# Optimization experiments

Measured on AMD Instinct MI355X. Metric: run time of the kernel, lower is better.

The kernel has to match this reference:

```python
import jax, jax.numpy as jnp
import numpy as np

LN_EPS = 1e-5

def _layer_norm(y):
    # elementwise_affine=False LayerNorm over last dim
    mu = jnp.mean(y, axis=-1, keepdims=True)
    var = jnp.var(y, axis=-1, keepdims=True)
    return (y - mu) / jnp.sqrt(var + LN_EPS)

def setup_inputs() -> dict:
    key = jax.random.key(0)
    k0, k1, k2, k3, k4 = jax.random.split(key, 5)
    N, D, D_qk, D_v, n_out = 8192, 1024, 128, 1024, 1024
    w_std = 0.02
    x = jax.random.normal(k0, (N, D), dtype=jnp.float32)
    Wq = jax.random.normal(k1, (D_qk, D), dtype=jnp.float32) * w_std
    Wk = jax.random.normal(k2, (D_qk, D), dtype=jnp.float32) * w_std
    Wv = jax.random.normal(k3, (D_v, D), dtype=jnp.float32) * w_std
    Wl = jax.random.normal(k4, (n_out, D), dtype=jnp.float32) * w_std
    return {"x": x, "Wq": Wq, "Wk": Wk, "Wv": Wv, "Wl": Wl}

def reference(x, Wq, Wk, Wv, Wl):
    # Faithful to source: scores are MULTIPLIED by sqrt(D_qk) (the variable
    # dq_sqrt_inv is np.sqrt(D_qk), applied multiplicatively).
    scale = jnp.sqrt(jnp.asarray(Wq.shape[0], dtype=x.dtype))
    q = x @ Wq.T              # [N, D_qk]
    k = x @ Wk.T              # [N, D_qk]
    v = x @ Wv.T              # [N, D_v]
    attn = jax.nn.softmax(scale * (q @ k.T), axis=-1)  # [N, N]
    sa = attn @ v             # [N, D_v]
    h = _layer_norm(x + sa)   # residual + LN1
    return _layer_norm(sa + h @ Wl.T)  # linear + residual + LN2
```

## Files before the change

### kernel.cpp

```cpp
#include <hip/hip_runtime.h>
#include <hip/hip_bf16.h>
#include <math.h>

#define N_TOK 8192
#define D_IN  1024
#define D_QK  128

typedef short bf16x8 __attribute__((ext_vector_type(8)));
typedef float f32x4 __attribute__((ext_vector_type(4)));
typedef unsigned short u16;
typedef u16 u16x8 __attribute__((ext_vector_type(8)));

static __device__ __forceinline__ u16 f2bf(float f) {
  __hip_bfloat16 b = __float2bfloat16(f);
  return *(u16*)&b;
}
static __device__ __forceinline__ float bf2f(u16 u) {
  __hip_bfloat16 b = *(__hip_bfloat16*)&u;
  return __bfloat162float(b);
}

static __device__ __forceinline__ void gload_lds16(const void* g, void* lds) {
  __builtin_amdgcn_global_load_lds(
      (const __attribute__((address_space(1))) unsigned int*)g,
      (__attribute__((address_space(3))) unsigned int*)lds, 16, 0, 0);
}

template <int F32OUT>
__global__ __launch_bounds__(256, 2) void gemm_mfma(const u16* __restrict__ A,
                                                    const u16* __restrict__ B,
                                                    void* __restrict__ Cv,
                                                    int M, int N, int K) {
  __shared__ __align__(16) u16 As[128 * 32];
  __shared__ __align__(16) u16 Bs[128 * 32];
  const int tid = threadIdx.x;
  const int w = tid >> 6, l = tid & 63;
  const int lr = l & 15, lg = l >> 4;
  const int m0 = blockIdx.y * 128, n0 = blockIdx.x * 128;
  const int wr = (w >> 1) * 64, wc = (w & 1) * 64;

  f32x4 acc[4][4];
#pragma unroll
  for (int m = 0; m < 4; ++m)
#pragma unroll
    for (int n = 0; n < 4; ++n) {
      f32x4 z = {0.f, 0.f, 0.f, 0.f};
      acc[m][n] = z;
    }

  const int ldsb0 = (w * 2 + 0) * 1024;
  const int ldsb1 = (w * 2 + 1) * 1024;
  const int srow0 = (w * 2 + 0) * 16 + (l >> 2);
  const int srow1 = (w * 2 + 1) * 16 + (l >> 2);
  const int scol = (l & 3) * 8;

  for (int kt = 0; kt < K; kt += 32) {
    gload_lds16(A + (size_t)(m0 + srow0) * K + kt + scol, (char*)As + ldsb0);
    gload_lds16(A + (size_t)(m0 + srow1) * K + kt + scol, (char*)As + ldsb1);
    gload_lds16(B + (size_t)(n0 + srow0) * K + kt + scol, (char*)Bs + ldsb0);
    gload_lds16(B + (size_t)(n0 + srow1) * K + kt + scol, (char*)Bs + ldsb1);
    __syncthreads();
    bf16x8 af[4], bfr[4];
#pragma unroll
    for (int m = 0; m < 4; ++m)
      af[m] = *(const bf16x8*)((char*)As + (wr + m * 16 + lr) * 64 + lg * 16);
#pragma unroll
    for (int n = 0; n < 4; ++n)
      bfr[n] = *(const bf16x8*)((char*)Bs + (wc + n * 16 + lr) * 64 + lg * 16);
#pragma unroll
    for (int m = 0; m < 4; ++m)
#pragma unroll
      for (int n = 0; n < 4; ++n)
        acc[m][n] = __builtin_amdgcn_mfma_f32_16x16x32_bf16(af[m], bfr[n], acc[m][n], 0, 0, 0);
    __syncthreads();
  }
#pragma unroll
  for (int m = 0; m < 4; ++m)
#pragma unroll
    for (int n = 0; n < 4; ++n)
#pragma unroll
      for (int r = 0; r < 4; ++r) {
        const size_t row = m0 + wr + m * 16 + lg * 4 + r;
        const size_t col = n0 + wc + n * 16 + lr;
        if (F32OUT)
          ((float*)Cv)[row * N + col] = acc[m][n][r];
        else
          ((u16*)Cv)[row * N + col] = f2bf(acc[m][n][r]);
      }
}

__global__ __launch_bounds__(256, 2) void gemm_hilo(
    const u16* __restrict__ Ah, const u16* __restrict__ Al,
    const u16* __restrict__ BhQ, const u16* __restrict__ BlQ,
    u16* __restrict__ ChQ, u16* __restrict__ ClQ,
    const u16* __restrict__ BhK, const u16* __restrict__ BlK,
    u16* __restrict__ ChK, u16* __restrict__ ClK, int K) {
  const bool isQ = (blockIdx.x == 0);
  const u16* Bh = isQ ? BhQ : BhK;
  const u16* Bl = isQ ? BlQ : BlK;
  u16* Ch = isQ ? ChQ : ChK;
  u16* Cl = isQ ? ClQ : ClK;
  const float scale = isQ ? 11.31370849898476f : 1.0f;
  __shared__ __align__(16) u16 Ahs[64 * 32], Als[64 * 32];
  __shared__ __align__(16) u16 Bhs[128 * 32], Bls[128 * 32];
  const int tid = threadIdx.x;
  const int w = tid >> 6, l = tid & 63;
  const int lr = l & 15, lg = l >> 4;
  const int m0 = blockIdx.y * 64;
  const int wc = w * 32;

  f32x4 acc[4][2];
#pragma unroll
  for (int m = 0; m < 4; ++m)
#pragma unroll
    for (int n = 0; n < 2; ++n) {
      f32x4 z = {0.f, 0.f, 0.f, 0.f};
      acc[m][n] = z;
    }

  const int arow = w * 16 + (l >> 2);
  const int brow0 = (w * 2 + 0) * 16 + (l >> 2);
  const int brow1 = (w * 2 + 1) * 16 + (l >> 2);
  const int scol = (l & 3) * 8;

  for (int kt = 0; kt < K; kt += 32) {
    gload_lds16(Ah + (size_t)(m0 + arow) * K + kt + scol, (char*)Ahs + w * 1024);
    gload_lds16(Al + (size_t)(m0 + arow) * K + kt + scol, (char*)Als + w * 1024);
    gload_lds16(Bh + (size_t)brow0 * K + kt + scol, (char*)Bhs + (w * 2 + 0) * 1024);
    gload_lds16(Bh + (size_t)brow1 * K + kt + scol, (char*)Bhs + (w * 2 + 1) * 1024);
    gload_lds16(Bl + (size_t)brow0 * K + kt + scol, (char*)Bls + (w * 2 + 0) * 1024);
    gload_lds16(Bl + (size_t)brow1 * K + kt + scol, (char*)Bls + (w * 2 + 1) * 1024);
    __syncthreads();
    bf16x8 afh[4], afl[4], bfh[2], bfl[2];
#pragma unroll
    for (int m = 0; m < 4; ++m) {
      afh[m] = *(const bf16x8*)((char*)Ahs + (m * 16 + lr) * 64 + lg * 16);
      afl[m] = *(const bf16x8*)((char*)Als + (m * 16 + lr) * 64 + lg * 16);
    }
#pragma unroll
    for (int n = 0; n < 2; ++n) {
      bfh[n] = *(const bf16x8*)((char*)Bhs + (wc + n * 16 + lr) * 64 + lg * 16);
      bfl[n] = *(const bf16x8*)((char*)Bls + (wc + n * 16 + lr) * 64 + lg * 16);
    }
#pragma unroll
    for (int m = 0; m < 4; ++m)
#pragma unroll
      for (int n = 0; n < 2; ++n) {
        acc[m][n] = __builtin_amdgcn_mfma_f32_16x16x32_bf16(afh[m], bfh[n], acc[m][n], 0, 0, 0);
        acc[m][n] = __builtin_amdgcn_mfma_f32_16x16x32_bf16(afh[m], bfl[n], acc[m][n], 0, 0, 0);
        acc[m][n] = __builtin_amdgcn_mfma_f32_16x16x32_bf16(afl[m], bfh[n], acc[m][n], 0, 0, 0);
      }
    __syncthreads();
  }
#pragma unroll
  for (int m = 0; m < 4; ++m)
#pragma unroll
    for (int n = 0; n < 2; ++n)
#pragma unroll
      for (int r = 0; r < 4; ++r) {
        const size_t row = m0 + m * 16 + lg * 4 + r;
        const size_t col = wc + n * 16 + lr;
        const float v = acc[m][n][r] * scale;
        const u16 h = f2bf(v);
        Ch[row * 128 + col] = h;
        Cl[row * 128 + col] = f2bf(v - bf2f(h));
      }
}

__global__ __launch_bounds__(256) void cvt_bf16(const float* __restrict__ in,
                                                u16* __restrict__ out) {
  const size_t idx = (size_t)blockIdx.x * 256 + threadIdx.x;
  const float4 a = ((const float4*)in)[idx * 2];
  const float4 b = ((const float4*)in)[idx * 2 + 1];
  u16x8 o;
  o[0] = f2bf(a.x); o[1] = f2bf(a.y); o[2] = f2bf(a.z); o[3] = f2bf(a.w);
  o[4] = f2bf(b.x); o[5] = f2bf(b.y); o[6] = f2bf(b.z); o[7] = f2bf(b.w);
  ((u16x8*)out)[idx] = o;
}

__global__ __launch_bounds__(256) void split_hl(const float* __restrict__ in,
                                                u16* __restrict__ hi,
                                                u16* __restrict__ lo) {
  const size_t idx = (size_t)blockIdx.x * 256 + threadIdx.x;
  const float4 v = ((const float4*)in)[idx];
  float f[4] = {v.x, v.y, v.z, v.w};
  u16 h[4], g[4];
#pragma unroll
  for (int i = 0; i < 4; ++i) {
    h[i] = f2bf(f[i]);
    g[i] = f2bf(f[i] - bf2f(h[i]));
  }
  ushort4 hv; hv.x = h[0]; hv.y = h[1]; hv.z = h[2]; hv.w = h[3];
  ushort4 gv; gv.x = g[0]; gv.y = g[1]; gv.z = g[2]; gv.w = g[3];
  ((ushort4*)hi)[idx] = hv;
  ((ushort4*)lo)[idx] = gv;
}

__global__ __launch_bounds__(256) void repack_k(const u16* __restrict__ krh,
                                                const u16* __restrict__ krl,
                                                u16* __restrict__ khT,
                                                u16* __restrict__ klT) {
  const int gid = blockIdx.x * 256 + threadIdx.x;
  const int f = gid >> 6, l = gid & 63;
  const int fn = f >> 2, fk = f & 3;
  const size_t src = (size_t)(fn * 16 + (l & 15)) * 128 + fk * 32 + (l >> 4) * 8;
  *(u16x8*)(khT + (size_t)f * 512 + l * 8) = *(const u16x8*)(krh + src);
  *(u16x8*)(klT + (size_t)f * 512 + l * 8) = *(const u16x8*)(krl + src);
}

__global__ __launch_bounds__(256) void repack_vt(const u16* __restrict__ vr,
                                                 u16* __restrict__ vt) {
  const int gid = blockIdx.x * 256 + threadIdx.x;
  const int f = gid >> 6, l = gid & 63;
  const int fn = f >> 8, fk = f & 255;
  const size_t src = (size_t)(fn * 16 + (l & 15)) * 8192 + fk * 32 + (l >> 4) * 8;
  *(u16x8*)(vt + (size_t)f * 512 + l * 8) = *(const u16x8*)(vr + src);
}

__global__ __launch_bounds__(512) __attribute__((amdgpu_waves_per_eu(2, 2)))
void flash_attn_mfma(const u16* __restrict__ qh, const u16* __restrict__ ql,
                     const u16* __restrict__ khT, const u16* __restrict__ klT,
                     const u16* __restrict__ vt, float* __restrict__ sa) {
  __shared__ __align__(16) u16 Qs[2 * 8192];
  __shared__ __align__(16) u16 P[64 * 128];
  __shared__ __align__(16) float pmax[64][12];
  __shared__ __align__(16) float lpart[64][12];
  __shared__ __align__(16) float facl[64];
  const int tid = threadIdx.x;
  const int w = tid >> 6, l = tid & 63;
  const int lr = l & 15, lg = l >> 4;
  const int q0 = blockIdx.y * 64;
  const int half = blockIdx.x;

  {
#pragma unroll
    for (int i = 0; i < 2; ++i) {
      const int e = i * 512 + tid;
      const int row = e >> 4, c16 = e & 15;
      const u16x8 hv = *(const u16x8*)(qh + (size_t)(q0 + row) * 128 + c16 * 8);
      const u16x8 lv = *(const u16x8*)(ql + (size_t)(q0 + row) * 128 + c16 * 8);
      const int b = (row * 256 + c16 * 16) ^ ((row & 7) << 4);
      *(u16x8*)((char*)Qs + b) = hv;
      *(u16x8*)((char*)Qs + 16384 + b) = lv;
    }
  }

  float mrun4[4] = {-INFINITY, -INFINITY, -INFINITY, -INFINITY};
  float lrun4[4] = {0.f, 0.f, 0.f, 0.f};

  f32x4 acc[4][4];
#pragma unroll
  for (int mt = 0; mt < 4; ++mt)
#pragma unroll
    for (int nt = 0; nt < 4; ++nt) {
      f32x4 z = {0.f, 0.f, 0.f, 0.f};
      acc[mt][nt] = z;
    }

  bf16x8 kfh[4], kfl[4];
#pragma unroll
  for (int ks = 0; ks < 4; ++ks) {
    kfh[ks] = *(const bf16x8*)(khT + ((size_t)w * 4 + ks) * 512 + l * 8);
    kfl[ks] = *(const bf16x8*)(klT + ((size_t)w * 4 + ks) * 512 + l * 8);
  }
  __syncthreads();

  const int vcol0 = half * 32 + w * 4;

  for (int t = 0; t < 64; ++t) {
    const int c = t * 4;
    f32x4 sfT[4];
#pragma unroll
    for (int mt = 0; mt < 4; ++mt) {
      f32x4 z = {0.f, 0.f, 0.f, 0.f};
      sfT[mt] = z;
    }
    __builtin_amdgcn_s_setprio(1);
#pragma unroll
    for (int ks = 0; ks < 4; ++ks)
#pragma unroll
      for (int mt = 0; mt < 4; ++mt) {
        const int b = ((mt * 16 + lr) * 256 + ks * 64 + lg * 16) ^ ((lr & 7) << 4);
        const bf16x8 qfh = *(const bf16x8*)((char*)Qs + b);
        const bf16x8 qfl = *(const bf16x8*)((char*)Qs + 16384 + b);
        sfT[mt] = __builtin_amdgcn_mfma_f32_16x16x32_bf16(kfh[ks], qfh, sfT[mt], 0, 0, 0);
        sfT[mt] = __builtin_amdgcn_mfma_f32_16x16x32_bf16(kfl[ks], qfh, sfT[mt], 0, 0, 0);
        sfT[mt] = __builtin_amdgcn_mfma_f32_16x16x32_bf16(kfh[ks], qfl, sfT[mt], 0, 0, 0);
      }
    __builtin_amdgcn_s_setprio(0);
    if (t < 63) {
#pragma unroll
      for (int ks = 0; ks < 4; ++ks) {
        kfh[ks] = *(const bf16x8*)(khT + ((size_t)((t + 1) * 8 + w) * 4 + ks) * 512 + l * 8);
        kfl[ks] = *(const bf16x8*)(klT + ((size_t)((t + 1) * 8 + w) * 4 + ks) * 512 + l * 8);
      }
    }
    bf16x8 vA[4], vB[4];
#pragma unroll
    for (int nt = 0; nt < 4; ++nt)
      vA[nt] = *(const bf16x8*)(vt + ((size_t)(vcol0 + nt) * 256 + c + 0) * 512 + l * 8);

    float wmax[4];
#pragma unroll
    for (int mt = 0; mt < 4; ++mt)
      wmax[mt] = fmaxf(fmaxf(sfT[mt][0], sfT[mt][1]), fmaxf(sfT[mt][2], sfT[mt][3]));
#pragma unroll
    for (int mt = 0; mt < 4; ++mt) {
      wmax[mt] = fmaxf(wmax[mt], __shfl_xor(wmax[mt], 16));
      wmax[mt] = fmaxf(wmax[mt], __shfl_xor(wmax[mt], 32));
    }
    if (lg == 0) {
#pragma unroll
      for (int mt = 0; mt < 4; ++mt) pmax[mt * 16 + lr][w] = wmax[mt];
    }
    __syncthreads();

    float mn4[4], fac4[4];
#pragma unroll
    for (int mt = 0; mt < 4; ++mt) {
      const int q = mt * 16 + lr;
      const f32x4 a = *(const f32x4*)&pmax[q][0];
      const f32x4 b = *(const f32x4*)&pmax[q][4];
      const float mx = fmaxf(fmaxf(fmaxf(a[0], a[1]), fmaxf(a[2], a[3])),
                             fmaxf(fmaxf(b[0], b[1]), fmaxf(b[2], b[3])));
      const float mn = fmaxf(mrun4[mt], mx);
      fac4[mt] = __expf(mrun4[mt] - mn);
      mn4[mt] = mn;
      mrun4[mt] = mn;
    }
    if (w == 0 && lg == 0) {
#pragma unroll
      for (int mt = 0; mt < 4; ++mt) facl[mt * 16 + lr] = fac4[mt];
    }
#pragma unroll
    for (int mt = 0; mt < 4; ++mt) {
      const float e0 = __expf(sfT[mt][0] - mn4[mt]);
      const float e1 = __expf(sfT[mt][1] - mn4[mt]);
      const float e2 = __expf(sfT[mt][2] - mn4[mt]);
      const float e3 = __expf(sfT[mt][3] - mn4[mt]);
      float tot = (e0 + e1) + (e2 + e3);
      tot += __shfl_xor(tot, 16);
      tot += __shfl_xor(tot, 32);
      lrun4[mt] = lrun4[mt] * fac4[mt] + tot;
      ushort4 pb;
      pb.x = f2bf(e0); pb.y = f2bf(e1); pb.z = f2bf(e2); pb.w = f2bf(e3);
      const int q = mt * 16 + lr;
      const int byte = (q * 256 + w * 32 + lg * 8) ^ ((lr & 7) << 4);
      *(ushort4*)((char*)P + byte) = pb;
    }
    __syncthreads();

#pragma unroll
    for (int mt = 0; mt < 4; ++mt) {
      const f32x4 f4 = *(const f32x4*)&facl[mt * 16 + lg * 4];
#pragma unroll
      for (int rr = 0; rr < 4; ++rr) {
        const float f = f4[rr];
        if (f != 1.0f) {
#pragma unroll
          for (int nt = 0; nt < 4; ++nt) acc[mt][nt][rr] *= f;
        }
      }
    }

#pragma unroll
    for (int ks = 0; ks < 4; ++ks) {
      bf16x8* nxt = (ks & 1) ? vA : vB;
      if (ks < 3) {
#pragma unroll
        for (int nt = 0; nt < 4; ++nt)
          nxt[nt] = *(const bf16x8*)(vt + ((size_t)(vcol0 + nt) * 256 + c + ks + 1) * 512 + l * 8);
      }
      const bf16x8* cur = (ks & 1) ? vB : vA;
      bf16x8 pf[4];
#pragma unroll
      for (int mt = 0; mt < 4; ++mt) {
        const int row = mt * 16 + lr;
        pf[mt] = *(const bf16x8*)((char*)P + ((row * 256 + ks * 64 + lg * 16) ^ ((lr & 7) << 4)));
      }
      __builtin_amdgcn_s_setprio(1);
#pragma unroll
      for (int mt = 0; mt < 4; ++mt)
#pragma unroll
        for (int nt = 0; nt < 4; ++nt)
          acc[mt][nt] = __builtin_amdgcn_mfma_f32_16x16x32_bf16(pf[mt], cur[nt], acc[mt][nt], 0, 0, 0);
      __builtin_amdgcn_s_setprio(0);
    }
  }
  if (lg == 0) {
#pragma unroll
    for (int mt = 0; mt < 4; ++mt) lpart[mt * 16 + lr][w] = lrun4[mt];
  }
  __syncthreads();
#pragma unroll
  for (int mt = 0; mt < 4; ++mt)
#pragma unroll
    for (int rr = 0; rr < 4; ++rr) {
      const int row = mt * 16 + lg * 4 + rr;
      const f32x4 a = *(const f32x4*)&lpart[row][0];
      const f32x4 b = *(const f32x4*)&lpart[row][4];
      const float inv =
          1.0f / (((a[0] + a[1]) + (a[2] + a[3])) + ((b[0] + b[1]) + (b[2] + b[3])));
#pragma unroll
      for (int nt = 0; nt < 4; ++nt)
        sa[(size_t)(q0 + row) * 1024 + half * 512 + w * 64 + nt * 16 + lr] =
            acc[mt][nt][rr] * inv;
    }
}

__global__ __launch_bounds__(256) void ln_add(const float* __restrict__ a,
                                              const float* __restrict__ b,
                                              float* __restrict__ o) {
  const int row = blockIdx.x;
  const int tid = threadIdx.x;
  const size_t base = (size_t)row * 256 + tid;
  const float4 av = ((const float4*)a)[base];
  const float4 bv = ((const float4*)b)[base];
  float4 y;
  y.x = av.x + bv.x; y.y = av.y + bv.y;
  y.z = av.z + bv.z; y.w = av.w + bv.w;
  float s1 = y.x + y.y + y.z + y.w;
  float s2 = y.x * y.x + y.y * y.y + y.z * y.z + y.w * y.w;
#pragma unroll
  for (int off = 32; off > 0; off >>= 1) {
    s1 += __shfl_xor(s1, off);
    s2 += __shfl_xor(s2, off);
  }
  __shared__ float r1[4];
  __shared__ float r2[4];
  if ((tid & 63) == 0) { r1[tid >> 6] = s1; r2[tid >> 6] = s2; }
  __syncthreads();
  s1 = r1[0] + r1[1] + r1[2] + r1[3];
  s2 = r2[0] + r2[1] + r2[2] + r2[3];
  const float mu = s1 * (1.0f / 1024.0f);
  const float var = s2 * (1.0f / 1024.0f) - mu * mu;
  const float rs = rsqrtf(var + 1e-5f);
  float4 ov;
  ov.x = (y.x - mu) * rs; ov.y = (y.y - mu) * rs;
  ov.z = (y.z - mu) * rs; ov.w = (y.w - mu) * rs;
  ((float4*)o)[base] = ov;
}

__global__ __launch_bounds__(256) void ln_add_bf16(const float* __restrict__ a,
                                                   const float* __restrict__ b,
                                                   u16* __restrict__ o) {
  const int row = blockIdx.x;
  const int tid = threadIdx.x;
  const size_t base = (size_t)row * 256 + tid;
  const float4 av = ((const float4*)a)[base];
  const float4 bv = ((const float4*)b)[base];
  float4 y;
  y.x = av.x + bv.x; y.y = av.y + bv.y;
  y.z = av.z + bv.z; y.w = av.w + bv.w;
  float s1 = y.x + y.y + y.z + y.w;
  float s2 = y.x * y.x + y.y * y.y + y.z * y.z + y.w * y.w;
#pragma unroll
  for (int off = 32; off > 0; off >>= 1) {
    s1 += __shfl_xor(s1, off);
    s2 += __shfl_xor(s2, off);
  }
  __shared__ float r1[4];
  __shared__ float r2[4];
  if ((tid & 63) == 0) { r1[tid >> 6] = s1; r2[tid >> 6] = s2; }
  __syncthreads();
  s1 = r1[0] + r1[1] + r1[2] + r1[3];
  s2 = r2[0] + r2[1] + r2[2] + r2[3];
  const float mu = s1 * (1.0f / 1024.0f);
  const float var = s2 * (1.0f / 1024.0f) - mu * mu;
  const float rs = rsqrtf(var + 1e-5f);
  ushort4 ov;
  ov.x = f2bf((y.x - mu) * rs); ov.y = f2bf((y.y - mu) * rs);
  ov.z = f2bf((y.z - mu) * rs); ov.w = f2bf((y.w - mu) * rs);
  ((ushort4*)o)[base] = ov;
}

extern "C" void kernel_launch(void* const* d_in, const int* in_sizes, int n_in,
                              void* d_out, int out_size, void* d_ws, size_t ws_size,
                              hipStream_t stream) {
  const float* x  = (const float*)d_in[0];
  const float* Wq = (const float*)d_in[1];
  const float* Wk = (const float*)d_in[2];
  const float* Wv = (const float*)d_in[3];
  const float* Wl = (const float*)d_in[4];
  float* out = (float*)d_out;

  char* w8 = (char*)d_ws;
  u16* xh  = (u16*)(w8 + (0ull << 20));
  u16* xl  = (u16*)(w8 + (16ull << 20));
  u16* khT = (u16*)(w8 + (16ull << 20));
  u16* klT = (u16*)(w8 + (18ull << 20));
  u16* vtr = (u16*)(w8 + (32ull << 20));
  u16* qh  = (u16*)(w8 + (32ull << 20));
  u16* ql  = (u16*)(w8 + (34ull << 20));
  u16* krh = (u16*)(w8 + (36ull << 20));
  u16* krl = (u16*)(w8 + (38ull << 20));
  u16* hb  = (u16*)(w8 + (32ull << 20));
  u16* vtt = (u16*)(w8 + (48ull << 20));
  float* sa = (float*)(w8 + (64ull << 20));
  u16* wqh = (u16*)(w8 + (92ull << 20));
  u16* wql = (u16*)(w8 + (92ull << 20) + (256ull << 10));
  u16* wkh = (u16*)(w8 + (92ull << 20) + (512ull << 10));
  u16* wkl = (u16*)(w8 + (92ull << 20) + (768ull << 10));
  u16* Wvb = (u16*)(w8 + (96ull << 20));
  u16* Wlb = (u16*)(w8 + (98ull << 20));

  split_hl<<<8192, 256, 0, stream>>>(x, xh, xl);
  cvt_bf16<<<512, 256, 0, stream>>>(Wv, Wvb);
  cvt_bf16<<<512, 256, 0, stream>>>(Wl, Wlb);
  gemm_mfma<0><<<dim3(64, 8), 256, 0, stream>>>(Wvb, xh, (void*)vtr, D_IN, N_TOK, D_IN);
  repack_vt<<<4096, 256, 0, stream>>>(vtr, vtt);
  split_hl<<<128, 256, 0, stream>>>(Wq, wqh, wql);
  split_hl<<<128, 256, 0, stream>>>(Wk, wkh, wkl);
  gemm_hilo<<<dim3(2, 128), 256, 0, stream>>>(xh, xl, wqh, wql, qh, ql,
                                              wkh, wkl, krh, krl, D_IN);
  repack_k<<<512, 256, 0, stream>>>(krh, krl, khT, klT);
  flash_attn_mfma<<<dim3(2, 128), 512, 0, stream>>>(qh, ql, khT, klT, vtt, sa);
  ln_add_bf16<<<N_TOK, 256, 0, stream>>>(x, sa, hb);
  gemm_mfma<1><<<dim3(8, 64), 256, 0, stream>>>(hb, Wlb, (void*)out, N_TOK, D_IN, D_IN);
  ln_add<<<N_TOK, 256, 0, stream>>>(sa, out, out);
}
```

Before: 398.0 us.

## Halve attention query tile to 32 rows, use 512 blocks with XCD-aware mapping

The flash attention kernel now handles 32 query rows per block instead of 64, doubling the grid to 512 one-dimensional blocks. Block indices are remapped so each XCD gets a fixed value half plus a contiguous range of query tiles, aiming for better L2 locality. Smaller tiles cut LDS and registers per block, which relaxes the occupancy limit and gives more blocks to fill 256 CUs. In exchange, each K and V tile is reloaded by twice as many blocks and there are fewer MFMAs per sync, so the per-iteration softmax and sync overhead weighs more.

```diff
diff --git a/kernel.cpp b/kernel.cpp
--- a/kernel.cpp
+++ b/kernel.cpp
@@ -217,40 +217,39 @@
   *(u16x8*)(vt + (size_t)f * 512 + l * 8) = *(const u16x8*)(vr + src);
 }
 
-__global__ __launch_bounds__(512) __attribute__((amdgpu_waves_per_eu(2, 2)))
+__global__ __launch_bounds__(512, 4)
 void flash_attn_mfma(const u16* __restrict__ qh, const u16* __restrict__ ql,
                      const u16* __restrict__ khT, const u16* __restrict__ klT,
                      const u16* __restrict__ vt, float* __restrict__ sa) {
-  __shared__ __align__(16) u16 Qs[2 * 8192];
-  __shared__ __align__(16) u16 P[64 * 128];
-  __shared__ __align__(16) float pmax[64][12];
-  __shared__ __align__(16) float lpart[64][12];
-  __shared__ __align__(16) float facl[64];
+  __shared__ __align__(16) u16 Qs[2 * 4096];
+  __shared__ __align__(16) u16 P[32 * 128];
+  __shared__ __align__(16) float pmax[32][12];
+  __shared__ __align__(16) float lpart[32][12];
+  __shared__ __align__(16) float facl[32];
   const int tid = threadIdx.x;
   const int w = tid >> 6, l = tid & 63;
   const int lr = l & 15, lg = l >> 4;
-  const int q0 = blockIdx.y * 64;
-  const int half = blockIdx.x;
+  const int n = blockIdx.x;
+  const int xcd = n & 7;
+  const int half = xcd & 1;
+  const int qb = (xcd >> 1) * 64 + (n >> 3);
+  const int q0 = qb * 32;
 
   {
-#pragma unroll
-    for (int i = 0; i < 2; ++i) {
-      const int e = i * 512 + tid;
-      const int row = e >> 4, c16 = e & 15;
-      const u16x8 hv = *(const u16x8*)(qh + (size_t)(q0 + row) * 128 + c16 * 8);
-      const u16x8 lv = *(const u16x8*)(ql + (size_t)(q0 + row) * 128 + c16 * 8);
-      const int b = (row * 256 + c16 * 16) ^ ((row & 7) << 4);
-      *(u16x8*)((char*)Qs + b) = hv;
-      *(u16x8*)((char*)Qs + 16384 + b) = lv;
-    }
-  }
-
-  float mrun4[4] = {-INFINITY, -INFINITY, -INFINITY, -INFINITY};
-  float lrun4[4] = {0.f, 0.f, 0.f, 0.f};
-
-  f32x4 acc[4][4];
-#pragma unroll
-  for (int mt = 0; mt < 4; ++mt)
+    const int row = tid >> 4, c16 = tid & 15;
+    const u16x8 hv = *(const u16x8*)(qh + (size_t)(q0 + row) * 128 + c16 * 8);
+    const u16x8 lv = *(const u16x8*)(ql + (size_t)(q0 + row) * 128 + c16 * 8);
+    const int b = (row * 256 + c16 * 16) ^ ((row & 7) << 4);
+    *(u16x8*)((char*)Qs + b) = hv;
+    *(u16x8*)((char*)Qs + 8192 + b) = lv;
+  }
+
+  float mrun2[2] = {-INFINITY, -INFINITY};
+  float lrun2[2] = {0.f, 0.f};
+
+  f32x4 acc[2][4];
+#pragma unroll
+  for (int mt = 0; mt < 2; ++mt)
 #pragma unroll
     for (int nt = 0; nt < 4; ++nt) {
       f32x4 z = {0.f, 0.f, 0.f, 0.f};
@@ -269,9 +268,9 @@
 
   for (int t = 0; t < 64; ++t) {
     const int c = t * 4;
-    f32x4 sfT[4];
-#pragma unroll
-    for (int mt = 0; mt < 4; ++mt) {
+    f32x4 sfT[2];
+#pragma unroll
+    for (int mt = 0; mt < 2; ++mt) {
       f32x4 z = {0.f, 0.f, 0.f, 0.f};
       sfT[mt] = z;
     }
@@ -279,10 +278,10 @@
 #pragma unroll
     for (int ks = 0; ks < 4; ++ks)
 #pragma unroll
-      for (int mt = 0; mt < 4; ++mt) {
+      for (int mt = 0; mt < 2; ++mt) {
         const int b = ((mt * 16 + lr) * 256 + ks * 64 + lg * 16) ^ ((lr & 7) << 4);
         const bf16x8 qfh = *(const bf16x8*)((char*)Qs + b);
-        const bf16x8 qfl = *(const bf16x8*)((char*)Qs + 16384 + b);
+        const bf16x8 qfl = *(const bf16x8*)((char*)Qs + 8192 + b);
         sfT[mt] = __builtin_amdgcn_mfma_f32_16x16x32_bf16(kfh[ks], qfh, sfT[mt], 0, 0, 0);
         sfT[mt] = __builtin_amdgcn_mfma_f32_16x16x32_bf16(kfl[ks], qfh, sfT[mt], 0, 0, 0);
         sfT[mt] = __builtin_amdgcn_mfma_f32_16x16x32_bf16(kfh[ks], qfl, sfT[mt], 0, 0, 0);
@@ -300,48 +299,46 @@
     for (int nt = 0; nt < 4; ++nt)
       vA[nt] = *(const bf16x8*)(vt + ((size_t)(vcol0 + nt) * 256 + c + 0) * 512 + l * 8);
 
-    float wmax[4];
-#pragma unroll
-    for (int mt = 0; mt < 4; ++mt)
+    float wmax[2];
+#pragma unroll
+    for (int mt = 0; mt < 2; ++mt) {
       wmax[mt] = fmaxf(fmaxf(sfT[mt][0], sfT[mt][1]), fmaxf(sfT[mt][2], sfT[mt][3]));
-#pragma unroll
-    for (int mt = 0; mt < 4; ++mt) {
       wmax[mt] = fmaxf(wmax[mt], __shfl_xor(wmax[mt], 16));
       wmax[mt] = fmaxf(wmax[mt], __shfl_xor(wmax[mt], 32));
     }
     if (lg == 0) {
 #pragma unroll
-      for (int mt = 0; mt < 4; ++mt) pmax[mt * 16 + lr][w] = wmax[mt];
+      for (int mt = 0; mt < 2; ++mt) pmax[mt * 16 + lr][w] = wmax[mt];
     }
     __syncthreads();
 
-    float mn4[4], fac4[4];
-#pragma unroll
-    for (int mt = 0; mt < 4; ++mt) {
+    float mn2[2], fac2[2];
+#pragma unroll
+    for (int mt = 0; mt < 2; ++mt) {
       const int q = mt * 16 + lr;
       const f32x4 a = *(const f32x4*)&pmax[q][0];
       const f32x4 b = *(const f32x4*)&pmax[q][4];
       const float mx = fmaxf(fmaxf(fmaxf(a[0], a[1]), fmaxf(a[2], a[3])),
                              fmaxf(fmaxf(b[0], b[1]), fmaxf(b[2], b[3])));
-      const float mn = fmaxf(mrun4[mt], mx);
-      fac4[mt] = __expf(mrun4[mt] - mn);
-      mn4[mt] = mn;
-      mrun4[mt] = mn;
+      const float mn = fmaxf(mrun2[mt], mx);
+      fac2[mt] = __expf(mrun2[mt] - mn);
+      mn2[mt] = mn;
+      mrun2[mt] = mn;
     }
     if (w == 0 && lg == 0) {
 #pragma unroll
-      for (int mt = 0; mt < 4; ++mt) facl[mt * 16 + lr] = fac4[mt];
-    }
-#pragma unroll
-    for (int mt = 0; mt < 4; ++mt) {
-      const float e0 = __expf(sfT[mt][0] - mn4[mt]);
-      const float e1 = __expf(sfT[mt][1] - mn4[mt]);
-      const float e2 = __expf(sfT[mt][2] - mn4[mt]);
-      const float e3 = __expf(sfT[mt][3] - mn4[mt]);
+      for (int mt = 0; mt < 2; ++mt) facl[mt * 16 + lr] = fac2[mt];
+    }
+#pragma unroll
+    for (int mt = 0; mt < 2; ++mt) {
+      const float e0 = __expf(sfT[mt][0] - mn2[mt]);
+      const float e1 = __expf(sfT[mt][1] - mn2[mt]);
+      const float e2 = __expf(sfT[mt][2] - mn2[mt]);
+      const float e3 = __expf(sfT[mt][3] - mn2[mt]);
       float tot = (e0 + e1) + (e2 + e3);
       tot += __shfl_xor(tot, 16);
       tot += __shfl_xor(tot, 32);
-      lrun4[mt] = lrun4[mt] * fac4[mt] + tot;
+      lrun2[mt] = lrun2[mt] * fac2[mt] + tot;
       ushort4 pb;
       pb.x = f2bf(e0); pb.y = f2bf(e1); pb.z = f2bf(e2); pb.w = f2bf(e3);
       const int q = mt * 16 + lr;
@@ -351,7 +348,7 @@
     __syncthreads();
 
 #pragma unroll
-    for (int mt = 0; mt < 4; ++mt) {
+    for (int mt = 0; mt < 2; ++mt) {
       const f32x4 f4 = *(const f32x4*)&facl[mt * 16 + lg * 4];
 #pragma unroll
       for (int rr = 0; rr < 4; ++rr) {
@@ -372,15 +369,15 @@
           nxt[nt] = *(const bf16x8*)(vt + ((size_t)(vcol0 + nt) * 256 + c + ks + 1) * 512 + l * 8);
       }
       const bf16x8* cur = (ks & 1) ? vB : vA;
-      bf16x8 pf[4];
-#pragma unroll
-      for (int mt = 0; mt < 4; ++mt) {
+      bf16x8 pf[2];
+#pragma unroll
+      for (int mt = 0; mt < 2; ++mt) {
         const int row = mt * 16 + lr;
         pf[mt] = *(const bf16x8*)((char*)P + ((row * 256 + ks * 64 + lg * 16) ^ ((lr & 7) << 4)));
       }
       __builtin_amdgcn_s_setprio(1);
 #pragma unroll
-      for (int mt = 0; mt < 4; ++mt)
+      for (int mt = 0; mt < 2; ++mt)
 #pragma unroll
         for (int nt = 0; nt < 4; ++nt)
           acc[mt][nt] = __builtin_amdgcn_mfma_f32_16x16x32_bf16(pf[mt], cur[nt], acc[mt][nt], 0, 0, 0);
@@ -389,11 +386,11 @@
   }
   if (lg == 0) {
 #pragma unroll
-    for (int mt = 0; mt < 4; ++mt) lpart[mt * 16 + lr][w] = lrun4[mt];
+    for (int mt = 0; mt < 2; ++mt) lpart[mt * 16 + lr][w] = lrun2[mt];
   }
   __syncthreads();
 #pragma unroll
-  for (int mt = 0; mt < 4; ++mt)
+  for (int mt = 0; mt < 2; ++mt)
 #pragma unroll
     for (int rr = 0; rr < 4; ++rr) {
       const int row = mt * 16 + lg * 4 + rr;
@@ -514,7 +511,7 @@
   gemm_hilo<<<dim3(2, 128), 256, 0, stream>>>(xh, xl, wqh, wql, qh, ql,
                                               wkh, wkl, krh, krl, D_IN);
   repack_k<<<512, 256, 0, stream>>>(krh, krl, khT, klT);
-  flash_attn_mfma<<<dim3(2, 128), 512, 0, stream>>>(qh, ql, khT, klT, vtt, sa);
+  flash_attn_mfma<<<512, 512, 0, stream>>>(qh, ql, khT, klT, vtt, sa);
   ln_add_bf16<<<N_TOK, 256, 0, stream>>>(x, sa, hb);
   gemm_mfma<1><<<dim3(8, 64), 256, 0, stream>>>(hb, Wlb, (void*)out, N_TOK, D_IN, D_IN);
   ln_add<<<N_TOK, 256, 0, stream>>>(sa, out, out);
```

Result: slower. 513.1 us (+28.9%).

## Use 16-wave flash-attention blocks with XCD-aware block mapping

Applied to the files above, without the earlier changes.

The flash-attention kernel now runs 1024 threads (16 waves) per block instead of 512. Each step covers 256 keys, with each wave computing 16 keys for the score pass and 2 V column tiles instead of 4. The P tile, max and sum buffers grow to match. The grid is flattened to 256 blocks and mapped so blocks sharing an XCD work on the same V half and neighbouring query blocks, which is meant to improve L2 reuse. The V-fragment prefetch is reordered into a two-deep ping-pong. The change trades fewer accumulators per wave for more waves hiding latency, at the cost of more cross-wave reduction work and 16-wave barriers.

```diff
diff --git a/kernel.cpp b/kernel.cpp
--- a/kernel.cpp
+++ b/kernel.cpp
@@ -217,42 +217,41 @@
   *(u16x8*)(vt + (size_t)f * 512 + l * 8) = *(const u16x8*)(vr + src);
 }
 
-__global__ __launch_bounds__(512) __attribute__((amdgpu_waves_per_eu(2, 2)))
+__global__ __launch_bounds__(1024) __attribute__((amdgpu_waves_per_eu(4, 4)))
 void flash_attn_mfma(const u16* __restrict__ qh, const u16* __restrict__ ql,
                      const u16* __restrict__ khT, const u16* __restrict__ klT,
                      const u16* __restrict__ vt, float* __restrict__ sa) {
   __shared__ __align__(16) u16 Qs[2 * 8192];
-  __shared__ __align__(16) u16 P[64 * 128];
-  __shared__ __align__(16) float pmax[64][12];
-  __shared__ __align__(16) float lpart[64][12];
+  __shared__ __align__(16) u16 P[64 * 256];
+  __shared__ __align__(16) float pmax[64][20];
+  __shared__ __align__(16) float lpart[64][20];
   __shared__ __align__(16) float facl[64];
   const int tid = threadIdx.x;
   const int w = tid >> 6, l = tid & 63;
   const int lr = l & 15, lg = l >> 4;
-  const int q0 = blockIdx.y * 64;
-  const int half = blockIdx.x;
+  const int n = blockIdx.x;
+  const int xcd = n & 7;
+  const int half = xcd & 1;
+  const int qb = (xcd >> 1) * 32 + (n >> 3);
+  const int q0 = qb * 64;
 
   {
-#pragma unroll
-    for (int i = 0; i < 2; ++i) {
-      const int e = i * 512 + tid;
-      const int row = e >> 4, c16 = e & 15;
-      const u16x8 hv = *(const u16x8*)(qh + (size_t)(q0 + row) * 128 + c16 * 8);
-      const u16x8 lv = *(const u16x8*)(ql + (size_t)(q0 + row) * 128 + c16 * 8);
-      const int b = (row * 256 + c16 * 16) ^ ((row & 7) << 4);
-      *(u16x8*)((char*)Qs + b) = hv;
-      *(u16x8*)((char*)Qs + 16384 + b) = lv;
-    }
+    const int row = tid >> 4, c16 = tid & 15;
+    const u16x8 hv = *(const u16x8*)(qh + (size_t)(q0 + row) * 128 + c16 * 8);
+    const u16x8 lv = *(const u16x8*)(ql + (size_t)(q0 + row) * 128 + c16 * 8);
+    const int b = (row * 256 + c16 * 16) ^ ((row & 7) << 4);
+    *(u16x8*)((char*)Qs + b) = hv;
+    *(u16x8*)((char*)Qs + 16384 + b) = lv;
   }
 
   float mrun4[4] = {-INFINITY, -INFINITY, -INFINITY, -INFINITY};
   float lrun4[4] = {0.f, 0.f, 0.f, 0.f};
 
-  f32x4 acc[4][4];
+  f32x4 acc[4][2];
 #pragma unroll
   for (int mt = 0; mt < 4; ++mt)
 #pragma unroll
-    for (int nt = 0; nt < 4; ++nt) {
+    for (int nt = 0; nt < 2; ++nt) {
       f32x4 z = {0.f, 0.f, 0.f, 0.f};
       acc[mt][nt] = z;
     }
@@ -260,15 +259,21 @@
   bf16x8 kfh[4], kfl[4];
 #pragma unroll
   for (int ks = 0; ks < 4; ++ks) {
-    kfh[ks] = *(const bf16x8*)(khT + ((size_t)w * 4 + ks) * 512 + l * 8);
-    kfl[ks] = *(const bf16x8*)(klT + ((size_t)w * 4 + ks) * 512 + l * 8);
+    kfh[ks] = *(const bf16x8*)(khT + ((size_t)(0 * 16 + w) * 4 + ks) * 512 + l * 8);
+    kfl[ks] = *(const bf16x8*)(klT + ((size_t)(0 * 16 + w) * 4 + ks) * 512 + l * 8);
   }
   __syncthreads();
 
-  const int vcol0 = half * 32 + w * 4;
-
-  for (int t = 0; t < 64; ++t) {
-    const int c = t * 4;
+  const int vc0 = half * 32 + w * 2;
+
+  for (int t = 0; t < 32; ++t) {
+    const int c = t * 8;
+    bf16x8 vA[2], vB[2];
+#pragma unroll
+    for (int nt = 0; nt < 2; ++nt) {
+      vA[nt] = *(const bf16x8*)(vt + ((size_t)(vc0 + nt) * 256 + c + 0) * 512 + l * 8);
+      vB[nt] = *(const bf16x8*)(vt + ((size_t)(vc0 + nt) * 256 + c + 1) * 512 + l * 8);
+    }
     f32x4 sfT[4];
 #pragma unroll
     for (int mt = 0; mt < 4; ++mt) {
@@ -288,24 +293,18 @@
         sfT[mt] = __builtin_amdgcn_mfma_f32_16x16x32_bf16(kfh[ks], qfl, sfT[mt], 0, 0, 0);
       }
     __builtin_amdgcn_s_setprio(0);
-    if (t < 63) {
+    if (t < 31) {
 #pragma unroll
       for (int ks = 0; ks < 4; ++ks) {
-        kfh[ks] = *(const bf16x8*)(khT + ((size_t)((t + 1) * 8 + w) * 4 + ks) * 512 + l * 8);
-        kfl[ks] = *(const bf16x8*)(klT + ((size_t)((t + 1) * 8 + w) * 4 + ks) * 512 + l * 8);
-      }
-    }
-    bf16x8 vA[4], vB[4];
-#pragma unroll
-    for (int nt = 0; nt < 4; ++nt)
-      vA[nt] = *(const bf16x8*)(vt + ((size_t)(vcol0 + nt) * 256 + c + 0) * 512 + l * 8);
+        kfh[ks] = *(const bf16x8*)(khT + ((size_t)((t + 1) * 16 + w) * 4 + ks) * 512 + l * 8);
+        kfl[ks] = *(const bf16x8*)(klT + ((size_t)((t + 1) * 16 + w) * 4 + ks) * 512 + l * 8);
+      }
+    }
 
     float wmax[4];
 #pragma unroll
-    for (int mt = 0; mt < 4; ++mt)
+    for (int mt = 0; mt < 4; ++mt) {
       wmax[mt] = fmaxf(fmaxf(sfT[mt][0], sfT[mt][1]), fmaxf(sfT[mt][2], sfT[mt][3]));
-#pragma unroll
-    for (int mt = 0; mt < 4; ++mt) {
       wmax[mt] = fmaxf(wmax[mt], __shfl_xor(wmax[mt], 16));
       wmax[mt] = fmaxf(wmax[mt], __shfl_xor(wmax[mt], 32));
     }
@@ -321,8 +320,12 @@
       const int q = mt * 16 + lr;
       const f32x4 a = *(const f32x4*)&pmax[q][0];
       const f32x4 b = *(const f32x4*)&pmax[q][4];
-      const float mx = fmaxf(fmaxf(fmaxf(a[0], a[1]), fmaxf(a[2], a[3])),
-                             fmaxf(fmaxf(b[0], b[1]), fmaxf(b[2], b[3])));
+      const f32x4 c2 = *(const f32x4*)&pmax[q][8];
+      const f32x4 d = *(const f32x4*)&pmax[q][12];
+      float mx = fmaxf(fmaxf(fmaxf(a[0], a[1]), fmaxf(a[2], a[3])),
+                       fmaxf(fmaxf(b[0], b[1]), fmaxf(b[2], b[3])));
+      mx = fmaxf(mx, fmaxf(fmaxf(fmaxf(c2[0], c2[1]), fmaxf(c2[2], c2[3])),
+                           fmaxf(fmaxf(d[0], d[1]), fmaxf(d[2], d[3]))));
       const float mn = fmaxf(mrun4[mt], mx);
       fac4[mt] = __expf(mrun4[mt] - mn);
       mn4[mt] = mn;
@@ -345,7 +348,7 @@
       ushort4 pb;
       pb.x = f2bf(e0); pb.y = f2bf(e1); pb.z = f2bf(e2); pb.w = f2bf(e3);
       const int q = mt * 16 + lr;
-      const int byte = (q * 256 + w * 32 + lg * 8) ^ ((lr & 7) << 4);
+      const int byte = (q * 512 + w * 32 + lg * 8) ^ ((q & 7) << 4);
       *(ushort4*)((char*)P + byte) = pb;
     }
     __syncthreads();
@@ -358,33 +361,30 @@
         const float f = f4[rr];
         if (f != 1.0f) {
 #pragma unroll
-          for (int nt = 0; nt < 4; ++nt) acc[mt][nt][rr] *= f;
+          for (int nt = 0; nt < 2; ++nt) acc[mt][nt][rr] *= f;
         }
       }
     }
 
 #pragma unroll
-    for (int ks = 0; ks < 4; ++ks) {
-      bf16x8* nxt = (ks & 1) ? vA : vB;
-      if (ks < 3) {
-#pragma unroll
-        for (int nt = 0; nt < 4; ++nt)
-          nxt[nt] = *(const bf16x8*)(vt + ((size_t)(vcol0 + nt) * 256 + c + ks + 1) * 512 + l * 8);
-      }
-      const bf16x8* cur = (ks & 1) ? vB : vA;
-      bf16x8 pf[4];
+    for (int ks = 0; ks < 8; ++ks) {
+      bf16x8* cur = (ks & 1) ? vB : vA;
+      __builtin_amdgcn_s_setprio(1);
 #pragma unroll
       for (int mt = 0; mt < 4; ++mt) {
         const int row = mt * 16 + lr;
-        pf[mt] = *(const bf16x8*)((char*)P + ((row * 256 + ks * 64 + lg * 16) ^ ((lr & 7) << 4)));
-      }
-      __builtin_amdgcn_s_setprio(1);
-#pragma unroll
-      for (int mt = 0; mt < 4; ++mt)
-#pragma unroll
-        for (int nt = 0; nt < 4; ++nt)
-          acc[mt][nt] = __builtin_amdgcn_mfma_f32_16x16x32_bf16(pf[mt], cur[nt], acc[mt][nt], 0, 0, 0);
+        const bf16x8 pf = *(const bf16x8*)((char*)P +
+            ((row * 512 + ks * 64 + lg * 16) ^ ((row & 7) << 4)));
+#pragma unroll
+        for (int nt = 0; nt < 2; ++nt)
+          acc[mt][nt] = __builtin_amdgcn_mfma_f32_16x16x32_bf16(pf, cur[nt], acc[mt][nt], 0, 0, 0);
+      }
       __builtin_amdgcn_s_setprio(0);
+      if (ks < 6) {
+#pragma unroll
+        for (int nt = 0; nt < 2; ++nt)
+          cur[nt] = *(const bf16x8*)(vt + ((size_t)(vc0 + nt) * 256 + c + ks + 2) * 512 + l * 8);
+      }
     }
   }
   if (lg == 0) {
@@ -399,11 +399,15 @@
       const int row = mt * 16 + lg * 4 + rr;
       const f32x4 a = *(const f32x4*)&lpart[row][0];
       const f32x4 b = *(const f32x4*)&lpart[row][4];
-      const float inv =
-          1.0f / (((a[0] + a[1]) + (a[2] + a[3])) + ((b[0] + b[1]) + (b[2] + b[3])));
-#pragma unroll
-      for (int nt = 0; nt < 4; ++nt)
-        sa[(size_t)(q0 + row) * 1024 + half * 512 + w * 64 + nt * 16 + lr] =
+      const f32x4 c2 = *(const f32x4*)&lpart[row][8];
+      const f32x4 d = *(const f32x4*)&lpart[row][12];
+      const float inv = 1.0f / ((((a[0] + a[1]) + (a[2] + a[3])) +
+                                 ((b[0] + b[1]) + (b[2] + b[3]))) +
+                                (((c2[0] + c2[1]) + (c2[2] + c2[3])) +
+                                 ((d[0] + d[1]) + (d[2] + d[3]))));
+#pragma unroll
+      for (int nt = 0; nt < 2; ++nt)
+        sa[(size_t)(q0 + row) * 1024 + half * 512 + (w * 2 + nt) * 16 + lr] =
             acc[mt][nt][rr] * inv;
     }
 }
@@ -514,7 +518,7 @@
   gemm_hilo<<<dim3(2, 128), 256, 0, stream>>>(xh, xl, wqh, wql, qh, ql,
                                               wkh, wkl, krh, krl, D_IN);
   repack_k<<<512, 256, 0, stream>>>(krh, krl, khT, klT);
-  flash_attn_mfma<<<dim3(2, 128), 512, 0, stream>>>(qh, ql, khT, klT, vtt, sa);
+  flash_attn_mfma<<<256, 1024, 0, stream>>>(qh, ql, khT, klT, vtt, sa);
   ln_add_bf16<<<N_TOK, 256, 0, stream>>>(x, sa, hb);
   gemm_mfma<1><<<dim3(8, 64), 256, 0, stream>>>(hb, Wlb, (void*)out, N_TOK, D_IN, D_IN);
   ln_add<<<N_TOK, 256, 0, stream>>>(sa, out, out);
```

Result: slower. 897.9 us (+125.6%).
